# Performance work log

Measured on AMD Instinct MI355X. Metric: run time of the kernel, lower is better.

The kernel has to match this reference:

```python
import jax, jax.numpy as jnp
import numpy as np

B, N, C = 4, 2048, 81
IMG_W, IMG_H = 1024.0, 800.0
SCORE_THRESH = 0.05
NMS_THRESH = 0.5
DETS_PER_IMG = 100
BBOX_XFORM_CLIP = float(np.log(1000.0 / 16.0))
WX, WY, WW, WH = 10.0, 10.0, 5.0, 5.0


def _make_boxes(key, n):
    k1, k2, k3, k4 = jax.random.split(key, 4)
    x1 = jax.random.uniform(k1, (n,)) * (IMG_W - 60.0)
    y1 = jax.random.uniform(k2, (n,)) * (IMG_H - 60.0)
    w = 10.0 + jax.random.uniform(k3, (n,)) * 300.0
    h = 10.0 + jax.random.uniform(k4, (n,)) * 300.0
    return jnp.stack([x1, y1, jnp.minimum(x1 + w, IMG_W - 1.0), jnp.minimum(y1 + h, IMG_H - 1.0)], axis=-1)


def setup_inputs() -> dict:
    key = jax.random.key(0)
    k1, k2, k3, k4 = jax.random.split(key, 4)
    return {
        "class_logits": jax.random.normal(k1, (B * N, C), jnp.float32),
        "box_regression": jax.random.normal(k2, (B * N, C * 8), jnp.float32) * 0.5,
        "left_proposals": _make_boxes(k3, B * N),
        "right_proposals": _make_boxes(k4, B * N),
    }


def decode(rel, boxes):
    widths = boxes[:, 2] - boxes[:, 0] + 1.0
    heights = boxes[:, 3] - boxes[:, 1] + 1.0
    ctr_x = boxes[:, 0] + 0.5 * widths
    ctr_y = boxes[:, 1] + 0.5 * heights
    dx = rel[:, 0::4] / WX
    dy = rel[:, 1::4] / WY
    dw = jnp.minimum(rel[:, 2::4] / WW, BBOX_XFORM_CLIP)
    dh = jnp.minimum(rel[:, 3::4] / WH, BBOX_XFORM_CLIP)
    pcx = dx * widths[:, None] + ctr_x[:, None]
    pcy = dy * heights[:, None] + ctr_y[:, None]
    pw = jnp.exp(dw) * widths[:, None]
    ph = jnp.exp(dh) * heights[:, None]
    x1 = pcx - 0.5 * pw
    y1 = pcy - 0.5 * ph
    x2 = pcx + 0.5 * pw - 1.0
    y2 = pcy + 0.5 * ph - 1.0
    return jnp.stack([x1, y1, x2, y2], axis=-1)  # [M, C, 4]


def clip_boxes(b):
    x1 = jnp.clip(b[..., 0], 0.0, IMG_W - 1.0)
    y1 = jnp.clip(b[..., 1], 0.0, IMG_H - 1.0)
    x2 = jnp.clip(b[..., 2], 0.0, IMG_W - 1.0)
    y2 = jnp.clip(b[..., 3], 0.0, IMG_H - 1.0)
    return jnp.stack([x1, y1, x2, y2], axis=-1)


def pairwise_iou(b):
    area = jnp.clip(b[:, 2] - b[:, 0] + 1.0, 0.0) * jnp.clip(b[:, 3] - b[:, 1] + 1.0, 0.0)
    lt = jnp.maximum(b[:, None, :2], b[None, :, :2])
    rb = jnp.minimum(b[:, None, 2:], b[None, :, 2:])
    wh = jnp.clip(rb - lt + 1.0, 0.0)
    inter = wh[..., 0] * wh[..., 1]
    return inter / jnp.maximum(area[:, None] + area[None, :] - inter, 1e-6)


def nms_keep(boxes, scores):
    # greedy NMS -> boolean keep mask (fixed shape)
    n = scores.shape[0]
    order = jnp.argsort(-scores)
    iou = pairwise_iou(boxes[order])
    idx = jnp.arange(n)
    def body(i, keep):
        sup = (iou[i] > NMS_THRESH) & keep[i] & (idx > i)
        return keep & (~sup)
    keep = jax.lax.fori_loop(0, n, body, jnp.ones((n,), bool))
    return jnp.zeros((n,), bool).at[order].set(keep)


def _per_image(prob, lb, rb):
    # prob [N,C], lb/rb [N,C,4]
    labels = jnp.argmax(prob, axis=-1)
    ar = jnp.arange(prob.shape[0])
    score = prob[ar, labels]
    lbox = lb[ar, labels]
    rbox = rb[ar, labels]
    valid = (labels >= 1) & (score > SCORE_THRESH)
    s = jnp.where(valid, score, -jnp.inf)
    keep = nms_keep(lbox, s) & nms_keep(rbox, s) & valid
    ms = jnp.where(keep, score, -jnp.inf)
    kth = jax.lax.top_k(ms, DETS_PER_IMG)[0][-1]
    keep = keep & (ms >= kth)
    return lbox, rbox, score, keep


def reference(class_logits, box_regression, left_proposals, right_proposals):
    prob = jax.nn.softmax(class_logits, axis=-1)  # [B*N, C]
    reg = box_regression.reshape(-1, C, 8)
    lb = clip_boxes(decode(reg[:, :, :4].reshape(-1, C * 4), left_proposals))
    rb = clip_boxes(decode(reg[:, :, 4:].reshape(-1, C * 4), right_proposals))
    prob = prob.reshape(B, N, C)
    lb = lb.reshape(B, N, C, 4)
    rb = rb.reshape(B, N, C, 4)
    lbox, rbox, score, keep = jax.vmap(_per_image)(prob, lb, rb)
    m = keep[..., None].astype(score.dtype)
    out = jnp.concatenate([lbox * m, rbox * m, jnp.where(keep, score, 0.0)[..., None]], axis=-1)
    return out  # [B, N, 9]
```

## Files before the change

### kernel.cpp

```cpp
#include <hip/hip_runtime.h>
#include <math.h>

#define NPROP 2048
#define NIMG 4
#define NCLS 81
#define REGW 648
#define SCORE_THRESH 0.05f
#define NMS_T 0.5f
#define DETS 100
#define XC 1023.0f
#define YC 799.0f
#define BBOX_CLIP 4.135166556742356f
#define NBIN 8192
#define SEL 320
#define MAXC 512
#define WRD 8
#define TRIP 2560

typedef unsigned long long u64;

__device__ __forceinline__ float areaf(float4 v) {
  return fmaxf(v.z - v.x + 1.0f, 0.0f) * fmaxf(v.w - v.y + 1.0f, 0.0f);
}
__device__ __forceinline__ bool iou_gt(float4 a, float aa, float4 b, float ba) {
  float ix1 = fmaxf(a.x, b.x), iy1 = fmaxf(a.y, b.y);
  float ix2 = fminf(a.z, b.z), iy2 = fminf(a.w, b.w);
  float iw = fmaxf(ix2 - ix1 + 1.0f, 0.0f);
  float ih = fmaxf(iy2 - iy1 + 1.0f, 0.0f);
  float inter = iw * ih;
  return inter > NMS_T * fmaxf(aa + ba - inter, 1e-6f);
}
__device__ __forceinline__ float score_from_v(unsigned v) {
  unsigned uu = ~v;
  unsigned bits = (uu & 0x80000000u) ? (uu & 0x7fffffffu) : ~uu;
  return __uint_as_float(bits);
}
__device__ __forceinline__ float4 decode_side(const float* __restrict__ reg,
                                              const float4* __restrict__ props,
                                              int grow, int ci, int isR) {
  const float* r = reg + (size_t)grow * REGW + ci * 8 + isR * 4;
  float4 P = props[grow];
  float w  = P.z - P.x + 1.0f;
  float h  = P.w - P.y + 1.0f;
  float cx = P.x + 0.5f * w;
  float cy = P.y + 0.5f * h;
  float dx = r[0] / 10.0f;
  float dy = r[1] / 10.0f;
  float dw = fminf(r[2] / 5.0f, BBOX_CLIP);
  float dh = fminf(r[3] / 5.0f, BBOX_CLIP);
  float pcx = dx * w + cx;
  float pcy = dy * h + cy;
  float pw = expf(dw) * w;
  float ph = expf(dh) * h;
  float4 o;
  o.x = fminf(fmaxf(pcx - 0.5f * pw, 0.0f), XC);
  o.y = fminf(fmaxf(pcy - 0.5f * ph, 0.0f), YC);
  o.z = fminf(fmaxf(pcx + 0.5f * pw - 1.0f, 0.0f), XC);
  o.w = fminf(fmaxf(pcy + 0.5f * ph - 1.0f, 0.0f), YC);
  return o;
}

__global__ __launch_bounds__(256) void score_kernel(
    const float* __restrict__ logits,
    unsigned* __restrict__ v32G, unsigned short* __restrict__ ci16G,
    float* __restrict__ out) {
  int row  = blockIdx.x * 4 + (threadIdx.x >> 6);
  int lane = threadIdx.x & 63;
  if (blockIdx.x < 72) {
    int g = blockIdx.x * 256 + threadIdx.x;
    ((float4*)out)[g] = make_float4(0.f, 0.f, 0.f, 0.f);
  }
  const float* lr = logits + (size_t)row * NCLS;
  float a = lr[lane];
  float b = (lane < NCLS - 64) ? lr[lane + 64] : -INFINITY;
  float v; int ci;
  if (b > a) { v = b; ci = lane + 64; } else { v = a; ci = lane; }
  for (int o = 32; o; o >>= 1) {
    float ov = __shfl_xor(v, o);
    int   oc = __shfl_xor(ci, o);
    if (ov > v || (ov == v && oc < ci)) { v = ov; ci = oc; }
  }
  float e = expf(a - v) + ((lane < NCLS - 64) ? expf(b - v) : 0.0f);
  for (int o = 32; o; o >>= 1) e += __shfl_xor(e, o);
  if (lane == 0) {
    float score = 1.0f / e;
    unsigned vv = 0xFFFFFFFFu;
    if (ci >= 1 && score > SCORE_THRESH) {
      unsigned uu = __float_as_uint(score);
      uu = (uu & 0x80000000u) ? ~uu : (uu | 0x80000000u);
      vv = ~uu;
    }
    v32G[row]  = vv;
    ci16G[row] = (unsigned short)ci;
  }
}

__global__ __launch_bounds__(1024) void nms8_kernel(
    const unsigned* __restrict__ v32G, const unsigned short* __restrict__ ci16G,
    const float* __restrict__ reg, const float* __restrict__ lp,
    const float* __restrict__ rp,
    unsigned short* __restrict__ srowG, unsigned* __restrict__ svG,
    float4* __restrict__ bxLG, float4* __restrict__ bxRG,
    u64* __restrict__ keepLG, u64* __restrict__ keepRG,
    int* __restrict__ C1G, int* __restrict__ C2G, int* __restrict__ flagG) {
  __shared__ int hist[NBIN];
  __shared__ u64 keys[MAXC];
  __shared__ unsigned short ssort[MAXC];
  __shared__ float4 bx[MAXC];
  __shared__ u64 mat[TRIP];
  __shared__ int wsum[16];
  __shared__ int Ts, cnts, ovf;
  int b = blockIdx.x >> 1, side = blockIdx.x & 1;
  int tid = threadIdx.x, ln = tid & 63, w = tid >> 6;
  const unsigned* v32 = v32G + b * NPROP;
  if (tid == 0) { Ts = NBIN - 1; cnts = 0; ovf = 0; }
  for (int i = tid; i < NBIN; i += 1024) hist[i] = 0;
  __syncthreads();
  for (int p = tid; p < NPROP; p += 1024) {
    unsigned v = v32[p];
    if (v != 0xFFFFFFFFu) atomicAdd(&hist[v >> 19], 1);
  }
  __syncthreads();
  {
    int base = tid * 8;
    int c[8]; int acc = 0;
#pragma unroll
    for (int k = 0; k < 8; ++k) { acc += hist[base + k]; c[k] = acc; }
    int tot = acc, v = tot;
#pragma unroll
    for (int o = 1; o < 64; o <<= 1) { int n = __shfl_up(v, o); if (ln >= o) v += n; }
    if (ln == 63) wsum[w] = v;
    __syncthreads();
    if (tid < 16) {
      int x = wsum[tid];
#pragma unroll
      for (int o = 1; o < 16; o <<= 1) { int n = __shfl_up(x, o); if (tid >= o) x += n; }
      wsum[tid] = x;
    }
    __syncthreads();
    int incl = ((w > 0) ? wsum[w - 1] : 0) + v;
    int off = incl - tot;
    int prev = off;
#pragma unroll
    for (int k = 0; k < 8; ++k) {
      int cur = off + c[k];
      if (cur >= SEL && prev < SEL) Ts = base + k;
      prev = cur;
    }
  }
  __syncthreads();
  int T = Ts, nvTot = wsum[15];
  for (int p = tid; p < NPROP; p += 1024) {
    unsigned v = v32[p];
    bool cand = (v != 0xFFFFFFFFu) && ((int)(v >> 19) <= T);
    u64 mb = __ballot(cand);
    int lpos = (int)__popcll(mb & ((1ull << ln) - 1ull));
    int wb = 0;
    if (ln == 0 && mb) wb = atomicAdd(&cnts, (int)__popcll(mb));
    wb = __shfl(wb, 0);
    if (cand) {
      int dst = wb + lpos;
      if (dst < MAXC) keys[dst] = ((u64)v << 16) | (unsigned)p;
      else ovf = 1;
    }
  }
  __syncthreads();
  int C1 = cnts;
  if (C1 > MAXC || ovf) {
    if (tid == 0) { flagG[b] = 1; C1G[b] = 0; C2G[b] = nvTot; }
    return;
  }
  if (tid == 0) { flagG[b] = 0; C1G[b] = C1; C2G[b] = nvTot; }
  if (tid < 256) {
    int i0 = tid, i1 = tid + 256;
    u64 k0 = (i0 < C1) ? keys[i0] : ~0ull;
    u64 k1 = (i1 < C1) ? keys[i1] : ~0ull;
    int r0 = 0, r1 = 0;
#pragma unroll 4
    for (int j = 0; j < C1; ++j) {
      u64 kj = keys[j];
      r0 += (kj < k0) ? 1 : 0;
      r1 += (kj < k1) ? 1 : 0;
    }
    if (i0 < C1) {
      unsigned short rw = (unsigned short)(k0 & 0xFFFFull);
      ssort[r0] = rw;
      srowG[b * MAXC + r0] = rw;
      svG[b * MAXC + r0]   = (unsigned)(k0 >> 16);
    }
    if (i1 < C1) {
      unsigned short rw = (unsigned short)(k1 & 0xFFFFull);
      ssort[r1] = rw;
      srowG[b * MAXC + r1] = rw;
      svG[b * MAXC + r1]   = (unsigned)(k1 >> 16);
    }
  }
  __syncthreads();

  int WRDu = (C1 + 63) >> 6;
  if (tid < MAXC) {
    float4 B = make_float4(0.f, 0.f, 0.f, 0.f);
    if (tid < C1) {
      int row  = ssort[tid];
      int grow = b * NPROP + row;
      int ci   = ci16G[grow];
      B = decode_side(reg, (const float4*)(side ? rp : lp), grow, ci, side);
      (side ? bxRG : bxLG)[b * MAXC + tid] = B;
    }
    bx[tid] = B;
  }
  __syncthreads();

  {
    int rb = w & 7, part = w >> 3;
    int r = rb * 64 + ln;
    float4 rbx = bx[r];
    float  rar = areaf(rbx);
    int tb = 0;
    for (int k = 0; k < rb; ++k) tb += ((8 - k) | 1);
    int Sw = (8 - rb) | 1;
    u64* myrow = &mat[tb * 64 + ln * Sw];
    for (int cw = rb + part; cw < WRDu; cw += 2) {
      u64 m = 0;
      const float4* cp = &bx[cw * 64];
#pragma unroll 8
      for (int c = 0; c < 64; ++c) {
        float4 cb = cp[c];
        float car = areaf(cb);
        if (iou_gt(rbx, rar, cb, car)) m |= (1ull << c);
      }
      if (cw == rb) m &= ~((2ull << ln) - 1ull);
      myrow[cw - rb] = m;
    }
  }
  __syncthreads();

  if (w == 0) {
    u64 A[WRD];
#pragma unroll
    for (int t = 0; t < WRD; ++t) {
      int b0 = t * 64;
      A[t] = (C1 >= b0 + 64) ? ~0ull : (C1 > b0 ? ((1ull << (C1 - b0)) - 1ull) : 0ull);
    }
    int tbase = 0;
#pragma unroll
    for (int wb = 0; wb < WRD; ++wb) {
      if (wb * 64 < C1) {
        const int Sw = (8 - wb) | 1;
        const u64* rowp = &mat[tbase];
        u64 aw = A[wb];
#pragma unroll
        for (int g = 0; g < 4; ++g) {
          u64 d[16];
#pragma unroll
          for (int k = 0; k < 16; ++k) d[k] = rowp[(g * 16 + k) * Sw];
#pragma unroll
          for (int k = 0; k < 16; ++k) {
            u64 msk = 0ull - ((aw >> (g * 16 + k)) & 1ull);
            aw &= ~(msk & d[k]);
          }
        }
        A[wb] = aw;
        bool alive = (aw >> ln) & 1ull;
#pragma unroll
        for (int t = wb + 1; t < WRD; ++t) {
          if (t * 64 < C1) {
            u64 x = alive ? rowp[ln * Sw + (t - wb)] : 0ull;
#pragma unroll
            for (int o = 1; o < 64; o <<= 1)
              x |= __shfl_xor((unsigned long long)x, o);
            A[t] &= ~x;
          }
        }
      }
      tbase += 64 * ((8 - wb) | 1);
    }
    if (ln == 0) {
      u64* kG = (side ? keepRG : keepLG) + b * WRD;
#pragma unroll
      for (int t = 0; t < WRD; ++t)
        if (t * 64 < C1) kG[t] = A[t];
    }
  }
}

struct SN {
  u64 keys[NPROP];
  unsigned short sidx[NPROP];
  unsigned v32s[NPROP];
  float4 bxL[MAXC], bxR[MAXC];
  float  arL[MAXC], arR[MAXC];
  u64 keepbL[NPROP / 64], keepbR[NPROP / 64];
  u64 rowmL[64], rowmR[64];
  float4 cbL[64], cbR[64];
  float  cbLa[64], cbRa[64];
  u64 aL, aR;
  int cnt, prevCount, done, ccL, ccR, needFB;
  unsigned kthV;
};

__device__ __forceinline__ float4 get_sboxN(SN* S, const float* reg,
                                            const float4* lp4, const float4* rp4,
                                            const unsigned short* ci16G,
                                            int b, int pos, int isR) {
  if (pos < MAXC) return isR ? S->bxR[pos] : S->bxL[pos];
  int row = S->sidx[pos];
  int grow = b * NPROP + row;
  return decode_side(reg, isR ? rp4 : lp4, grow, ci16G[grow], isR);
}

__global__ __launch_bounds__(1024) void finale_fallback_kernel(
    const float* __restrict__ reg, const float* __restrict__ lp,
    const float* __restrict__ rp, const unsigned* __restrict__ v32G,
    const unsigned short* __restrict__ ci16G,
    const u64* __restrict__ keepLG, const u64* __restrict__ keepRG,
    const unsigned* __restrict__ svG, const unsigned short* __restrict__ srowG,
    const float4* __restrict__ bxLG, const float4* __restrict__ bxRG,
    const int* __restrict__ C1G, const int* __restrict__ C2G,
    float* __restrict__ out) {
  __shared__ SN S;
  int b = blockIdx.x, tid = threadIdx.x, ln = tid & 63, w = tid >> 6;
  float* ob = out + (size_t)b * NPROP * 9;

  if (w == 0) {
    int C1 = C1G[b];
    int before = 0;
    unsigned kth = 0;
    for (int wb = 0; wb * 64 < C1; ++wb) {
      u64 m = keepLG[b * WRD + wb] & keepRG[b * WRD + wb];
      int pos = wb * 64 + ln;
      bool bit = (m >> ln) & 1ull;
      int rank = before + (int)__popcll(m & ((1ull << ln) - 1ull));
      unsigned vA = svG[b * MAXC + pos];
      u64 selm = __ballot(bit && rank == DETS - 1);
      if (selm) kth = __shfl(vA, __ffsll(selm) - 1);
      bool qual = bit && (rank < DETS || vA == kth);
      if (qual) {
        int row = srowG[b * MAXC + pos];
        float4 L = bxLG[b * MAXC + pos], R = bxRG[b * MAXC + pos];
        float* orow = ob + row * 9;
        orow[0]=L.x; orow[1]=L.y; orow[2]=L.z; orow[3]=L.w;
        orow[4]=R.x; orow[5]=R.y; orow[6]=R.z; orow[7]=R.w;
        orow[8]=score_from_v(vA);
      }
      before += (int)__popcll(m);
    }
    if (ln == 0) {
      S.needFB = (before < DETS && C2G[b] > C1) ? 1 : 0;
      S.cnt = 0; S.prevCount = 0; S.done = 0; S.kthV = 0u;
    }
  }
  __syncthreads();
  if (!S.needFB) return;

  const float4* lp4 = (const float4*)lp;
  const float4* rp4 = (const float4*)rp;
  float4* ob4 = (float4*)ob;
  float4 z4 = make_float4(0.f, 0.f, 0.f, 0.f);
  for (int i = tid; i < NPROP * 9 / 4; i += 1024) ob4[i] = z4;
  for (int p = tid; p < NPROP; p += 1024) {
    unsigned v = v32G[b * NPROP + p];
    S.v32s[p] = v;
    bool cand = (v != 0xFFFFFFFFu);
    u64 mb = __ballot(cand);
    int lpos = (int)__popcll(mb & ((1ull << ln) - 1ull));
    int wb = 0;
    if (ln == 0 && mb) wb = atomicAdd(&S.cnt, (int)__popcll(mb));
    wb = __shfl(wb, 0);
    if (cand) S.keys[wb + lpos] = ((u64)v << 16) | (unsigned)p;
  }
  __syncthreads();
  int C2 = S.cnt;
  int CbEnd = (C2 + 63) & ~63;
  {
    int i0 = tid, i1 = tid + 1024;
    u64 k0 = (i0 < C2) ? S.keys[i0] : ~0ull;
    u64 k1 = (i1 < C2) ? S.keys[i1] : ~0ull;
    int r0 = 0, r1 = 0;
#pragma unroll 4
    for (int j = 0; j < C2; ++j) {
      u64 kj = S.keys[j];
      r0 += (kj < k0) ? 1 : 0;
      r1 += (kj < k1) ? 1 : 0;
    }
    if (i0 < C2) S.sidx[r0] = (unsigned short)(k0 & 0xFFFFull);
    if (i1 < C2) S.sidx[r1] = (unsigned short)(k1 & 0xFFFFull);
  }
  for (int i = C2 + tid; i < CbEnd; i += 1024) S.sidx[i] = 0;
  for (int wd = tid; wd < NPROP / 64; wd += 1024) {
    int b0 = wd << 6;
    u64 mf = 0ull;
    if (C2 >= b0 + 64) mf = ~0ull;
    else if (C2 > b0)  mf = (1ull << (C2 - b0)) - 1ull;
    S.keepbL[wd] = mf; S.keepbR[wd] = mf;
  }
  __syncthreads();
  {
    int lim = min(CbEnd, MAXC);
    for (int i = tid; i < lim; i += 1024) {
      if (i < C2) {
        int row = S.sidx[i];
        int grow = b * NPROP + row;
        int ci = ci16G[grow];
        float4 L = decode_side(reg, lp4, grow, ci, 0);
        float4 R = decode_side(reg, lp4 == rp4 ? lp4 : rp4, grow, ci, 1);
        S.bxL[i] = L; S.arL[i] = areaf(L);
        S.bxR[i] = R; S.arR[i] = areaf(R);
      } else {
        S.bxL[i] = z4; S.arL[i] = 1.0f;
        S.bxR[i] = z4; S.arR[i] = 1.0f;
      }
    }
  }
  __syncthreads();
  for (int base = 0; base < CbEnd; base += 64) {
    {
      int isR = (w >= 8);
      float4 cbx = get_sboxN(&S, reg, lp4, rp4, ci16G, b, base + ln, isR);
      float car = (base + ln < MAXC) ? (isR ? S.arR[base + ln] : S.arL[base + ln])
                                     : areaf(cbx);
      int w8 = w & 7;
#pragma unroll
      for (int k = 0; k < 8; ++k) {
        int row = w8 * 8 + k;
        float4 rbx;
        rbx.x = __shfl(cbx.x, row); rbx.y = __shfl(cbx.y, row);
        rbx.z = __shfl(cbx.z, row); rbx.w = __shfl(cbx.w, row);
        float rar = __shfl(car, row);
        bool bit = (ln > row) && iou_gt(rbx, rar, cbx, car);
        u64 bal = __ballot(bit);
        if (ln == 0) { if (isR) S.rowmR[row] = bal; else S.rowmL[row] = bal; }
      }
    }
    __syncthreads();
    if (tid < 128) {
      int isR = (tid >= 64);
      u64* km = isR ? S.keepbR : S.keepbL;
      u64* rm = isR ? S.rowmR  : S.rowmL;
      u64 a = km[base >> 6];
#pragma unroll
      for (int j = 0; j < 64; ++j)
        a &= ~((0ull - ((a >> j) & 1ull)) & rm[j]);
      if (ln == 0) {
        km[base >> 6] = a;
        if (isR) { S.aR = a; S.ccR = __popcll(a); }
        else     { S.aL = a; S.ccL = __popcll(a); }
      }
      if ((a >> ln) & 1ull) {
        int pos = __popcll(a & ((1ull << ln) - 1ull));
        float4 v = get_sboxN(&S, reg, lp4, rp4, ci16G, b, base + ln, isR);
        if (isR) { S.cbR[pos] = v; S.cbRa[pos] = areaf(v); }
        else     { S.cbL[pos] = v; S.cbLa[pos] = areaf(v); }
      }
    }
    __syncthreads();
    if (w == 0) {
      u64 m = S.aL & S.aR;
      int before = S.prevCount;
      bool bit = (m >> ln) & 1ull;
      int rank = before + (int)__popcll(m & ((1ull << ln) - 1ull));
      int row = S.sidx[base + ln];
      unsigned vA = S.v32s[row];
      u64 selm = __ballot(bit && rank == DETS - 1);
      unsigned keffV = S.kthV;
      if (selm) keffV = __shfl(vA, __ffsll(selm) - 1);
      bool qual = bit && (rank < DETS || vA == keffV);
      if (qual) {
        float4 L = get_sboxN(&S, reg, lp4, rp4, ci16G, b, base + ln, 0);
        float4 R = get_sboxN(&S, reg, lp4, rp4, ci16G, b, base + ln, 1);
        float s = score_from_v(vA);
        float* orow = ob + row * 9;
        orow[0]=L.x; orow[1]=L.y; orow[2]=L.z; orow[3]=L.w;
        orow[4]=R.x; orow[5]=R.y; orow[6]=R.z; orow[7]=R.w;
        orow[8]=s;
      }
      if (ln == 0) {
        if (selm) S.kthV = keffV;
        int nc = before + (int)__popcll(m);
        S.prevCount = nc;
        if (nc >= DETS) {
          int nxt = base + 64;
          bool cont = false;
          if (nxt < C2) cont = (S.v32s[S.sidx[nxt]] == keffV);
          if (!cont) S.done = 1;
        }
      }
    } else {
      int cL = S.ccL, cR = S.ccR;
      if ((cL | cR) != 0) {
        for (int p = base + 64 + (tid - 64); p < CbEnd; p += 960) {
          float4 mbL = get_sboxN(&S, reg, lp4, rp4, ci16G, b, p, 0);
          float al = (p < MAXC) ? S.arL[p] : areaf(mbL);
          bool supL = false;
          for (int q = 0; q < cL; ++q)
            supL = supL || iou_gt(mbL, al, S.cbL[q], S.cbLa[q]);
          if (supL) atomicAnd(&S.keepbL[p >> 6], ~(1ull << (p & 63)));
          float4 mbR = get_sboxN(&S, reg, lp4, rp4, ci16G, b, p, 1);
          float ar_ = (p < MAXC) ? S.arR[p] : areaf(mbR);
          bool supR = false;
          for (int q = 0; q < cR; ++q)
            supR = supR || iou_gt(mbR, ar_, S.cbR[q], S.cbRa[q]);
          if (supR) atomicAnd(&S.keepbR[p >> 6], ~(1ull << (p & 63)));
        }
      }
    }
    __syncthreads();
    if (S.done) break;
  }
}

extern "C" void kernel_launch(void* const* d_in, const int* in_sizes, int n_in,
                              void* d_out, int out_size, void* d_ws, size_t ws_size,
                              hipStream_t stream) {
  const float* logits = (const float*)d_in[0];
  const float* reg    = (const float*)d_in[1];
  const float* lprop  = (const float*)d_in[2];
  const float* rprop  = (const float*)d_in[3];
  float* out = (float*)d_out;

  char* ws = (char*)d_ws;
  unsigned*       v32G   = (unsigned*)(ws + 0);
  unsigned short* ci16G  = (unsigned short*)(ws + 32768);
  unsigned short* srowG  = (unsigned short*)(ws + 49152);
  unsigned*       svG    = (unsigned*)(ws + 53248);
  float4*         bxLG   = (float4*)(ws + 61440);
  float4*         bxRG   = (float4*)(ws + 94208);
  u64*            keepLG = (u64*)(ws + 126976);
  u64*            keepRG = (u64*)(ws + 127232);
  int*            C1G    = (int*)(ws + 127488);
  int*            C2G    = (int*)(ws + 127504);
  int*            flagG  = (int*)(ws + 127520);

  score_kernel<<<NIMG * NPROP / 4, 256,  0, stream>>>(logits, v32G, ci16G, out);
  nms8_kernel <<<2 * NIMG,         1024, 0, stream>>>(v32G, ci16G, reg, lprop, rprop,
                                                      srowG, svG, bxLG, bxRG,
                                                      keepLG, keepRG, C1G, C2G, flagG);
  finale_fallback_kernel<<<NIMG,   1024, 0, stream>>>(reg, lprop, rprop, v32G, ci16G,
                                                      keepLG, keepRG, svG, srowG,
                                                      bxLG, bxRG, C1G, C2G, out);
}
```

Measured before the change: 123.3 us.

## Fuse NMS into finale kernel, predecode boxes in score kernel, shrink histogram

The per-side NMS kernel is merged with the finale/fallback kernel, so one launch is removed. The two side blocks of each image coordinate through a global done counter with spin-waiting. Box decoding for every row moves into the score kernel, which writes full decoded-box arrays that the NMS stage gathers. The 8192-bin threshold histogram is replaced by a 128-bin clamped histogram scanned by a single wave. The trade-offs are extra global writes of all decoded boxes, a reliance on both blocks of an image being resident at once for the spin-wait, and coarser bins that may select more candidates or overflow more often.

```diff
diff --git a/kernel.cpp b/kernel.cpp
--- a/kernel.cpp
+++ b/kernel.cpp
@@ -11,7 +11,8 @@
 #define XC 1023.0f
 #define YC 799.0f
 #define BBOX_CLIP 4.135166556742356f
-#define NBIN 8192
+#define HBIN 128
+#define HOFF 2048
 #define SEL 320
 #define MAXC 512
 #define WRD 8
@@ -61,15 +62,18 @@
 }
 
 __global__ __launch_bounds__(256) void score_kernel(
-    const float* __restrict__ logits,
+    const float* __restrict__ logits, const float* __restrict__ reg,
+    const float* __restrict__ lp, const float* __restrict__ rp,
     unsigned* __restrict__ v32G, unsigned short* __restrict__ ci16G,
-    float* __restrict__ out) {
+    float4* __restrict__ bxAllL, float4* __restrict__ bxAllR,
+    int* __restrict__ doneG, float* __restrict__ out) {
   int row  = blockIdx.x * 4 + (threadIdx.x >> 6);
   int lane = threadIdx.x & 63;
   if (blockIdx.x < 72) {
     int g = blockIdx.x * 256 + threadIdx.x;
     ((float4*)out)[g] = make_float4(0.f, 0.f, 0.f, 0.f);
   }
+  if (blockIdx.x == 100 && threadIdx.x < NIMG) doneG[threadIdx.x] = 0;
   const float* lr = logits + (size_t)row * NCLS;
   float a = lr[lane];
   float b = (lane < NCLS - 64) ? lr[lane + 64] : -INFINITY;
@@ -92,195 +96,8 @@
     }
     v32G[row]  = vv;
     ci16G[row] = (unsigned short)ci;
-  }
-}
-
-__global__ __launch_bounds__(1024) void nms8_kernel(
-    const unsigned* __restrict__ v32G, const unsigned short* __restrict__ ci16G,
-    const float* __restrict__ reg, const float* __restrict__ lp,
-    const float* __restrict__ rp,
-    unsigned short* __restrict__ srowG, unsigned* __restrict__ svG,
-    float4* __restrict__ bxLG, float4* __restrict__ bxRG,
-    u64* __restrict__ keepLG, u64* __restrict__ keepRG,
-    int* __restrict__ C1G, int* __restrict__ C2G, int* __restrict__ flagG) {
-  __shared__ int hist[NBIN];
-  __shared__ u64 keys[MAXC];
-  __shared__ unsigned short ssort[MAXC];
-  __shared__ float4 bx[MAXC];
-  __shared__ u64 mat[TRIP];
-  __shared__ int wsum[16];
-  __shared__ int Ts, cnts, ovf;
-  int b = blockIdx.x >> 1, side = blockIdx.x & 1;
-  int tid = threadIdx.x, ln = tid & 63, w = tid >> 6;
-  const unsigned* v32 = v32G + b * NPROP;
-  if (tid == 0) { Ts = NBIN - 1; cnts = 0; ovf = 0; }
-  for (int i = tid; i < NBIN; i += 1024) hist[i] = 0;
-  __syncthreads();
-  for (int p = tid; p < NPROP; p += 1024) {
-    unsigned v = v32[p];
-    if (v != 0xFFFFFFFFu) atomicAdd(&hist[v >> 19], 1);
-  }
-  __syncthreads();
-  {
-    int base = tid * 8;
-    int c[8]; int acc = 0;
-#pragma unroll
-    for (int k = 0; k < 8; ++k) { acc += hist[base + k]; c[k] = acc; }
-    int tot = acc, v = tot;
-#pragma unroll
-    for (int o = 1; o < 64; o <<= 1) { int n = __shfl_up(v, o); if (ln >= o) v += n; }
-    if (ln == 63) wsum[w] = v;
-    __syncthreads();
-    if (tid < 16) {
-      int x = wsum[tid];
-#pragma unroll
-      for (int o = 1; o < 16; o <<= 1) { int n = __shfl_up(x, o); if (tid >= o) x += n; }
-      wsum[tid] = x;
-    }
-    __syncthreads();
-    int incl = ((w > 0) ? wsum[w - 1] : 0) + v;
-    int off = incl - tot;
-    int prev = off;
-#pragma unroll
-    for (int k = 0; k < 8; ++k) {
-      int cur = off + c[k];
-      if (cur >= SEL && prev < SEL) Ts = base + k;
-      prev = cur;
-    }
-  }
-  __syncthreads();
-  int T = Ts, nvTot = wsum[15];
-  for (int p = tid; p < NPROP; p += 1024) {
-    unsigned v = v32[p];
-    bool cand = (v != 0xFFFFFFFFu) && ((int)(v >> 19) <= T);
-    u64 mb = __ballot(cand);
-    int lpos = (int)__popcll(mb & ((1ull << ln) - 1ull));
-    int wb = 0;
-    if (ln == 0 && mb) wb = atomicAdd(&cnts, (int)__popcll(mb));
-    wb = __shfl(wb, 0);
-    if (cand) {
-      int dst = wb + lpos;
-      if (dst < MAXC) keys[dst] = ((u64)v << 16) | (unsigned)p;
-      else ovf = 1;
-    }
-  }
-  __syncthreads();
-  int C1 = cnts;
-  if (C1 > MAXC || ovf) {
-    if (tid == 0) { flagG[b] = 1; C1G[b] = 0; C2G[b] = nvTot; }
-    return;
-  }
-  if (tid == 0) { flagG[b] = 0; C1G[b] = C1; C2G[b] = nvTot; }
-  if (tid < 256) {
-    int i0 = tid, i1 = tid + 256;
-    u64 k0 = (i0 < C1) ? keys[i0] : ~0ull;
-    u64 k1 = (i1 < C1) ? keys[i1] : ~0ull;
-    int r0 = 0, r1 = 0;
-#pragma unroll 4
-    for (int j = 0; j < C1; ++j) {
-      u64 kj = keys[j];
-      r0 += (kj < k0) ? 1 : 0;
-      r1 += (kj < k1) ? 1 : 0;
-    }
-    if (i0 < C1) {
-      unsigned short rw = (unsigned short)(k0 & 0xFFFFull);
-      ssort[r0] = rw;
-      srowG[b * MAXC + r0] = rw;
-      svG[b * MAXC + r0]   = (unsigned)(k0 >> 16);
-    }
-    if (i1 < C1) {
-      unsigned short rw = (unsigned short)(k1 & 0xFFFFull);
-      ssort[r1] = rw;
-      srowG[b * MAXC + r1] = rw;
-      svG[b * MAXC + r1]   = (unsigned)(k1 >> 16);
-    }
-  }
-  __syncthreads();
-
-  int WRDu = (C1 + 63) >> 6;
-  if (tid < MAXC) {
-    float4 B = make_float4(0.f, 0.f, 0.f, 0.f);
-    if (tid < C1) {
-      int row  = ssort[tid];
-      int grow = b * NPROP + row;
-      int ci   = ci16G[grow];
-      B = decode_side(reg, (const float4*)(side ? rp : lp), grow, ci, side);
-      (side ? bxRG : bxLG)[b * MAXC + tid] = B;
-    }
-    bx[tid] = B;
-  }
-  __syncthreads();
-
-  {
-    int rb = w & 7, part = w >> 3;
-    int r = rb * 64 + ln;
-    float4 rbx = bx[r];
-    float  rar = areaf(rbx);
-    int tb = 0;
-    for (int k = 0; k < rb; ++k) tb += ((8 - k) | 1);
-    int Sw = (8 - rb) | 1;
-    u64* myrow = &mat[tb * 64 + ln * Sw];
-    for (int cw = rb + part; cw < WRDu; cw += 2) {
-      u64 m = 0;
-      const float4* cp = &bx[cw * 64];
-#pragma unroll 8
-      for (int c = 0; c < 64; ++c) {
-        float4 cb = cp[c];
-        float car = areaf(cb);
-        if (iou_gt(rbx, rar, cb, car)) m |= (1ull << c);
-      }
-      if (cw == rb) m &= ~((2ull << ln) - 1ull);
-      myrow[cw - rb] = m;
-    }
-  }
-  __syncthreads();
-
-  if (w == 0) {
-    u64 A[WRD];
-#pragma unroll
-    for (int t = 0; t < WRD; ++t) {
-      int b0 = t * 64;
-      A[t] = (C1 >= b0 + 64) ? ~0ull : (C1 > b0 ? ((1ull << (C1 - b0)) - 1ull) : 0ull);
-    }
-    int tbase = 0;
-#pragma unroll
-    for (int wb = 0; wb < WRD; ++wb) {
-      if (wb * 64 < C1) {
-        const int Sw = (8 - wb) | 1;
-        const u64* rowp = &mat[tbase];
-        u64 aw = A[wb];
-#pragma unroll
-        for (int g = 0; g < 4; ++g) {
-          u64 d[16];
-#pragma unroll
-          for (int k = 0; k < 16; ++k) d[k] = rowp[(g * 16 + k) * Sw];
-#pragma unroll
-          for (int k = 0; k < 16; ++k) {
-            u64 msk = 0ull - ((aw >> (g * 16 + k)) & 1ull);
-            aw &= ~(msk & d[k]);
-          }
-        }
-        A[wb] = aw;
-        bool alive = (aw >> ln) & 1ull;
-#pragma unroll
-        for (int t = wb + 1; t < WRD; ++t) {
-          if (t * 64 < C1) {
-            u64 x = alive ? rowp[ln * Sw + (t - wb)] : 0ull;
-#pragma unroll
-            for (int o = 1; o < 64; o <<= 1)
-              x |= __shfl_xor((unsigned long long)x, o);
-            A[t] &= ~x;
-          }
-        }
-      }
-      tbase += 64 * ((8 - wb) | 1);
-    }
-    if (ln == 0) {
-      u64* kG = (side ? keepRG : keepLG) + b * WRD;
-#pragma unroll
-      for (int t = 0; t < WRD; ++t)
-        if (t * 64 < C1) kG[t] = A[t];
-    }
+    bxAllL[row] = decode_side(reg, (const float4*)lp, row, ci, 0);
+    bxAllR[row] = decode_side(reg, (const float4*)rp, row, ci, 1);
   }
 }
 
@@ -309,24 +126,196 @@
   return decode_side(reg, isR ? rp4 : lp4, grow, ci16G[grow], isR);
 }
 
-__global__ __launch_bounds__(1024) void finale_fallback_kernel(
+__global__ __launch_bounds__(1024) void nms_finale_kernel(
+    const unsigned* __restrict__ v32G, const unsigned short* __restrict__ ci16G,
     const float* __restrict__ reg, const float* __restrict__ lp,
-    const float* __restrict__ rp, const unsigned* __restrict__ v32G,
-    const unsigned short* __restrict__ ci16G,
-    const u64* __restrict__ keepLG, const u64* __restrict__ keepRG,
-    const unsigned* __restrict__ svG, const unsigned short* __restrict__ srowG,
-    const float4* __restrict__ bxLG, const float4* __restrict__ bxRG,
-    const int* __restrict__ C1G, const int* __restrict__ C2G,
-    float* __restrict__ out) {
+    const float* __restrict__ rp,
+    const float4* __restrict__ bxAllL, const float4* __restrict__ bxAllR,
+    unsigned short* __restrict__ srowG, unsigned* __restrict__ svG,
+    float4* __restrict__ bxLG, float4* __restrict__ bxRG,
+    u64* __restrict__ keepLG, u64* __restrict__ keepRG,
+    int* __restrict__ doneG, float* __restrict__ out) {
+  __shared__ int hist[HBIN];
+  __shared__ u64 keys[MAXC];
+  __shared__ unsigned short ssort[MAXC];
+  __shared__ float4 bx[MAXC];
+  __shared__ u64 mat[TRIP];
+  __shared__ int Ts, cnts, nv_sh;
   __shared__ SN S;
-  int b = blockIdx.x, tid = threadIdx.x, ln = tid & 63, w = tid >> 6;
+  int b = blockIdx.x >> 1, side = blockIdx.x & 1;
+  int tid = threadIdx.x, ln = tid & 63, w = tid >> 6;
+  const unsigned* v32 = v32G + b * NPROP;
   float* ob = out + (size_t)b * NPROP * 9;
 
+  if (tid == 0) { Ts = HBIN - 1; cnts = 0; }
+  if (tid < HBIN) hist[tid] = 0;
+  __syncthreads();
+  for (int p = tid; p < NPROP; p += 1024) {
+    unsigned v = v32[p];
+    if (v != 0xFFFFFFFFu) {
+      int bin = min(max((int)(v >> 19) - HOFF, 0), HBIN - 1);
+      atomicAdd(&hist[bin], 1);
+    }
+  }
+  __syncthreads();
   if (w == 0) {
-    int C1 = C1G[b];
+    int b0 = hist[2 * ln], b1 = hist[2 * ln + 1];
+    int s = b0 + b1;
+    int incl = s;
+#pragma unroll
+    for (int o = 1; o < 64; o <<= 1) { int n = __shfl_up(incl, o); if (ln >= o) incl += n; }
+    int off = incl - s;
+    int c0 = off + b0, c1 = off + s;
+    if      (c0 >= SEL && off < SEL) Ts = 2 * ln;
+    else if (c1 >= SEL && c0  < SEL) Ts = 2 * ln + 1;
+    if (ln == 63) nv_sh = incl;
+  }
+  __syncthreads();
+  int T = Ts, nvTot = nv_sh;
+  for (int p = tid; p < NPROP; p += 1024) {
+    unsigned v = v32[p];
+    bool cand = false;
+    if (v != 0xFFFFFFFFu) {
+      int bin = min(max((int)(v >> 19) - HOFF, 0), HBIN - 1);
+      cand = (bin <= T);
+    }
+    u64 mb = __ballot(cand);
+    int lpos = (int)__popcll(mb & ((1ull << ln) - 1ull));
+    int wb = 0;
+    if (ln == 0 && mb) wb = atomicAdd(&cnts, (int)__popcll(mb));
+    wb = __shfl(wb, 0);
+    if (cand) {
+      int dst = wb + lpos;
+      if (dst < MAXC) keys[dst] = ((u64)v << 16) | (unsigned)p;
+    }
+  }
+  __syncthreads();
+  int C1 = cnts;
+  bool okfast = (C1 <= MAXC);
+  int C1f = okfast ? C1 : 0;
+
+  if (okfast && C1 > 0) {
+    if (tid < 256) {
+      int i0 = tid, i1 = tid + 256;
+      u64 k0 = (i0 < C1) ? keys[i0] : ~0ull;
+      u64 k1 = (i1 < C1) ? keys[i1] : ~0ull;
+      int r0 = 0, r1 = 0;
+#pragma unroll 4
+      for (int j = 0; j < C1; ++j) {
+        u64 kj = keys[j];
+        r0 += (kj < k0) ? 1 : 0;
+        r1 += (kj < k1) ? 1 : 0;
+      }
+      if (i0 < C1) {
+        unsigned short rw = (unsigned short)(k0 & 0xFFFFull);
+        ssort[r0] = rw; srowG[b * MAXC + r0] = rw;
+        svG[b * MAXC + r0] = (unsigned)(k0 >> 16);
+      }
+      if (i1 < C1) {
+        unsigned short rw = (unsigned short)(k1 & 0xFFFFull);
+        ssort[r1] = rw; srowG[b * MAXC + r1] = rw;
+        svG[b * MAXC + r1] = (unsigned)(k1 >> 16);
+      }
+    }
+    __syncthreads();
+    if (tid < MAXC) {
+      float4 B = make_float4(0.f, 0.f, 0.f, 0.f);
+      if (tid < C1) {
+        int row = ssort[tid];
+        B = (side ? bxAllR : bxAllL)[b * NPROP + row];
+        (side ? bxRG : bxLG)[b * MAXC + tid] = B;
+      }
+      bx[tid] = B;
+    }
+    __syncthreads();
+    int WRDu = (C1 + 63) >> 6;
+    {
+      int rb = w & 7, part = w >> 3;
+      int r = rb * 64 + ln;
+      float4 rbx = bx[r];
+      float  rar = areaf(rbx);
+      int tb = 0;
+      for (int k = 0; k < rb; ++k) tb += ((8 - k) | 1);
+      int Sw = (8 - rb) | 1;
+      u64* myrow = &mat[tb * 64 + ln * Sw];
+      for (int cw = rb + part; cw < WRDu; cw += 2) {
+        u64 m = 0;
+        const float4* cp = &bx[cw * 64];
+#pragma unroll 8
+        for (int c = 0; c < 64; ++c) {
+          float4 cb = cp[c];
+          float car = areaf(cb);
+          if (iou_gt(rbx, rar, cb, car)) m |= (1ull << c);
+        }
+        if (cw == rb) m &= ~((2ull << ln) - 1ull);
+        myrow[cw - rb] = m;
+      }
+    }
+    __syncthreads();
+    if (w == 0) {
+      u64 A[WRD];
+#pragma unroll
+      for (int t = 0; t < WRD; ++t) {
+        int b0 = t * 64;
+        A[t] = (C1 >= b0 + 64) ? ~0ull : (C1 > b0 ? ((1ull << (C1 - b0)) - 1ull) : 0ull);
+      }
+      int tbase = 0;
+#pragma unroll
+      for (int wb = 0; wb < WRD; ++wb) {
+        if (wb * 64 < C1) {
+          const int Sw = (8 - wb) | 1;
+          const u64* rowp = &mat[tbase];
+          u64 aw = A[wb];
+#pragma unroll
+          for (int g = 0; g < 4; ++g) {
+            u64 d[16];
+#pragma unroll
+            for (int k = 0; k < 16; ++k) d[k] = rowp[(g * 16 + k) * Sw];
+#pragma unroll
+            for (int k = 0; k < 16; ++k) {
+              u64 msk = 0ull - ((aw >> (g * 16 + k)) & 1ull);
+              aw &= ~(msk & d[k]);
+            }
+          }
+          A[wb] = aw;
+          bool alive = (aw >> ln) & 1ull;
+#pragma unroll
+          for (int t = wb + 1; t < WRD; ++t) {
+            if (t * 64 < C1) {
+              u64 x = alive ? rowp[ln * Sw + (t - wb)] : 0ull;
+#pragma unroll
+              for (int o = 1; o < 64; o <<= 1)
+                x |= __shfl_xor((unsigned long long)x, o);
+              A[t] &= ~x;
+            }
+          }
+        }
+        tbase += 64 * ((8 - wb) | 1);
+      }
+      if (ln == 0) {
+        u64* kG = (side ? keepRG : keepLG) + b * WRD;
+#pragma unroll
+        for (int t = 0; t < WRD; ++t)
+          if (t * 64 < C1) kG[t] = A[t];
+      }
+    }
+  }
+  __threadfence();
+  __syncthreads();
+  if (tid == 0) atomicAdd(doneG + b, 1);
+  if (side == 1) return;
+
+  if (tid == 0) {
+    while (__hip_atomic_load(doneG + b, __ATOMIC_ACQUIRE, __HIP_MEMORY_SCOPE_AGENT) < 2)
+      __builtin_amdgcn_s_sleep(8);
+  }
+  __syncthreads();
+  __threadfence();
+
+  if (w == 0) {
     int before = 0;
     unsigned kth = 0;
-    for (int wb = 0; wb * 64 < C1; ++wb) {
+    for (int wb = 0; wb * 64 < C1f; ++wb) {
       u64 m = keepLG[b * WRD + wb] & keepRG[b * WRD + wb];
       int pos = wb * 64 + ln;
       bool bit = (m >> ln) & 1ull;
@@ -346,7 +335,7 @@
       before += (int)__popcll(m);
     }
     if (ln == 0) {
-      S.needFB = (before < DETS && C2G[b] > C1) ? 1 : 0;
+      S.needFB = (before < DETS && nvTot > C1f) ? 1 : 0;
       S.cnt = 0; S.prevCount = 0; S.done = 0; S.kthV = 0u;
     }
   }
@@ -403,7 +392,7 @@
         int grow = b * NPROP + row;
         int ci = ci16G[grow];
         float4 L = decode_side(reg, lp4, grow, ci, 0);
-        float4 R = decode_side(reg, lp4 == rp4 ? lp4 : rp4, grow, ci, 1);
+        float4 R = decode_side(reg, rp4, grow, ci, 1);
         S.bxL[i] = L; S.arL[i] = areaf(L);
         S.bxR[i] = R; S.arR[i] = areaf(R);
       } else {
@@ -527,15 +516,15 @@
   float4*         bxRG   = (float4*)(ws + 94208);
   u64*            keepLG = (u64*)(ws + 126976);
   u64*            keepRG = (u64*)(ws + 127232);
-  int*            C1G    = (int*)(ws + 127488);
-  int*            C2G    = (int*)(ws + 127504);
-  int*            flagG  = (int*)(ws + 127520);
-
-  score_kernel<<<NIMG * NPROP / 4, 256,  0, stream>>>(logits, v32G, ci16G, out);
-  nms8_kernel <<<2 * NIMG,         1024, 0, stream>>>(v32G, ci16G, reg, lprop, rprop,
-                                                      srowG, svG, bxLG, bxRG,
-                                                      keepLG, keepRG, C1G, C2G, flagG);
-  finale_fallback_kernel<<<NIMG,   1024, 0, stream>>>(reg, lprop, rprop, v32G, ci16G,
-                                                      keepLG, keepRG, svG, srowG,
-                                                      bxLG, bxRG, C1G, C2G, out);
-}
+  int*            doneG  = (int*)(ws + 127488);
+  float4*         bxAllL = (float4*)(ws + 131072);
+  float4*         bxAllR = (float4*)(ws + 262144);
+
+  score_kernel<<<NIMG * NPROP / 4, 256,  0, stream>>>(logits, reg, lprop, rprop,
+                                                      v32G, ci16G, bxAllL, bxAllR,
+                                                      doneG, out);
+  nms_finale_kernel<<<2 * NIMG,    1024, 0, stream>>>(v32G, ci16G, reg, lprop, rprop,
+                                                      bxAllL, bxAllR, srowG, svG,
+                                                      bxLG, bxRG, keepLG, keepRG,
+                                                      doneG, out);
+}
```

Result: slower. 128.5 us (+4.2%).
